# Optimization experiments

Measured on AMD Instinct MI355X. Metric: run time of the kernel, lower is better.

The kernel has to match this reference:

```python
import jax, jax.numpy as jnp
import numpy as np

HS = 1024      # hidden_size
NH = 16        # num_heads
HD = HS // NH  # head_dim = 64
WS = 24        # window_size
GWS = 8        # global_window_size
THETA = 10000.0
EPS = 1e-6


def _rope_tables():
    # matches Sam3ViTRotaryEmbedding with end_x=end_y=WS, scale=GWS/WS
    scale = GWS / WS
    freqs = 1.0 / THETA ** (np.arange(0, HD, 4)[: HD // 4].astype(np.float32) / HD)  # [HD//4]
    flat = np.arange(WS * WS)
    x_pos = (flat % WS).astype(np.float32) * scale
    y_pos = (flat // WS).astype(np.float32) * scale
    f = np.concatenate([np.outer(x_pos, freqs), np.outer(y_pos, freqs)], axis=-1)  # [S, HD//2]
    f = np.repeat(f, 2, axis=-1)  # repeat_interleave(2, dim=-1) -> [S, HD]
    return jnp.asarray(np.cos(f)), jnp.asarray(np.sin(f))


def _rotate_pairwise(x):
    shp = x.shape
    x = x.reshape(*shp[:-1], -1, 2)
    x1, x2 = x[..., 0], x[..., 1]
    return jnp.stack((-x2, x1), axis=-1).reshape(shp)


def _ln(x, g, b):
    m = x.mean(-1, keepdims=True)
    v = x.var(-1, keepdims=True)
    return (x - m) * jax.lax.rsqrt(v + EPS) * g + b


def setup_inputs() -> dict:
    key = jax.random.key(0)
    ks = jax.random.split(key, 8)
    B, H, W = 2, 72, 72
    s = 0.02
    inp = {
        "hidden_states": jax.random.normal(ks[0], (B, H, W, HS), jnp.float32),
        "ln1_g": jnp.ones((HS,), jnp.float32), "ln1_b": jnp.zeros((HS,), jnp.float32),
        "wq": jax.random.normal(ks[1], (HS, HS), jnp.float32) * s, "bq": jnp.zeros((HS,), jnp.float32),
        "wk": jax.random.normal(ks[2], (HS, HS), jnp.float32) * s, "bk": jnp.zeros((HS,), jnp.float32),
        "wv": jax.random.normal(ks[3], (HS, HS), jnp.float32) * s, "bv": jnp.zeros((HS,), jnp.float32),
        "wo": jax.random.normal(ks[4], (HS, HS), jnp.float32) * s, "bo": jnp.zeros((HS,), jnp.float32),
        "ln2_g": jnp.ones((HS,), jnp.float32), "ln2_b": jnp.zeros((HS,), jnp.float32),
        "w1": jax.random.normal(ks[5], (HS, 4 * HS), jnp.float32) * s, "b1": jnp.zeros((4 * HS,), jnp.float32),
        "w2": jax.random.normal(ks[6], (4 * HS, HS), jnp.float32) * s, "b2": jnp.zeros((HS,), jnp.float32),
    }
    return inp


def reference(hidden_states, ln1_g, ln1_b, wq, bq, wk, bk, wv, bv, wo, bo,
              ln2_g, ln2_b, w1, b1, w2, b2):
    B, H, W, C = hidden_states.shape
    residual = hidden_states
    x = _ln(hidden_states, ln1_g, ln1_b)

    # window partition: [B,H,W,C] -> [B*nW, S, C]  (H,W divisible by WS -> no pad)
    nh, nw = H // WS, W // WS
    xw = x.reshape(B, nh, WS, nw, WS, C).transpose(0, 1, 3, 2, 4, 5).reshape(-1, WS * WS, C)
    Bn, S = xw.shape[0], WS * WS

    q = (xw @ wq + bq).reshape(Bn, S, NH, HD).transpose(0, 2, 1, 3)  # [Bn,NH,S,HD]
    k = (xw @ wk + bk).reshape(Bn, S, NH, HD).transpose(0, 2, 1, 3)
    v = (xw @ wv + bv).reshape(Bn, S, NH, HD).transpose(0, 2, 1, 3)

    cos, sin = _rope_tables()  # [S, HD]
    q = q * cos + _rotate_pairwise(q) * sin
    k = k * cos + _rotate_pairwise(k) * sin

    attn = jax.nn.softmax(jnp.einsum('bhqd,bhkd->bhqk', q, k) * HD ** -0.5, axis=-1)
    o = jnp.einsum('bhqk,bhkd->bhqd', attn, v).transpose(0, 2, 1, 3).reshape(Bn, S, C)
    o = o @ wo + bo

    # window unpartition: [B*nW, S, C] -> [B,H,W,C]
    o = o.reshape(B, nh, nw, WS, WS, C).transpose(0, 1, 3, 2, 4, 5).reshape(B, H, W, C)

    x = residual + o
    y = _ln(x, ln2_g, ln2_b)
    y = jax.nn.gelu(y @ w1 + b1, approximate=False) @ w2 + b2
    return x + y
```

## Files before the change

kernel.cpp:

```cpp
#include <hip/hip_runtime.h>
#include <hip/hip_bf16.h>

#define DI __device__ __forceinline__

typedef short bf16x8 __attribute__((ext_vector_type(8)));
typedef float f32x4 __attribute__((ext_vector_type(4)));

typedef __attribute__((address_space(3))) unsigned lds_u32;
typedef __attribute__((address_space(1))) const unsigned g_u32;

DI void gload16(const void* g, void* lds) {
  __builtin_amdgcn_global_load_lds((g_u32*)g, (lds_u32*)lds, 16, 0, 0);
}

DI unsigned short bf16bits(float f) {
  __hip_bfloat16 h = __float2bfloat16(f);
  return *(unsigned short*)&h;
}

DI float gelu_fast(float v) {
  const float v2 = v * v;
  const float u = v * __builtin_fmaf(0.0356774081f, v2, 0.7978845608f);
  const float a = fabsf(u);
  const float e2 = __expf(-2.0f * a);
  const float r = __builtin_amdgcn_rcpf(1.0f + e2);
  float t = __builtin_fmaf(-2.0f * e2, r, 1.0f);
  t = copysignf(t, u);
  const float h = 0.5f * v;
  return __builtin_fmaf(h, t, h);
}

__global__ __launch_bounds__(256)
void wtrans_kernel(const float* __restrict__ w, __hip_bfloat16* __restrict__ wt,
                   int K, int N) {
  __shared__ float tile[32][33];
  const int nb = blockIdx.x * 32, kb = blockIdx.y * 32;
  const int tx = threadIdx.x & 31, ty = threadIdx.x >> 5;
#pragma unroll
  for (int i = 0; i < 4; ++i)
    tile[ty + i * 8][tx] = w[(size_t)(kb + ty + i * 8) * N + nb + tx];
  __syncthreads();
#pragma unroll
  for (int i = 0; i < 4; ++i)
    wt[(size_t)(nb + ty + i * 8) * K + kb + tx] = __float2bfloat16(tile[tx][ty + i * 8]);
}

__global__ void tables_kernel(float* __restrict__ cost, float* __restrict__ sint) {
  const int s = blockIdx.x;
  const int d = threadIdx.x;
  const int j = d >> 1;
  const float pos = (j < 16) ? (float)(s % 24) * (1.0f / 3.0f)
                             : (float)(s / 24) * (1.0f / 3.0f);
  const int fi = j & 15;
  const float freq = powf(10000.0f, -(float)fi * (1.0f / 16.0f));
  const float a = pos * freq;
  cost[s * 64 + d] = cosf(a);
  sint[s * 64 + d] = sinf(a);
}

__global__ __launch_bounds__(256)
void ln_kernel(const float* __restrict__ in, const float* __restrict__ g,
               const float* __restrict__ b, __hip_bfloat16* __restrict__ out) {
  const int t = blockIdx.x, tid = threadIdx.x;
  const float4 x = *(const float4*)(in + (size_t)t * 1024 + tid * 4);
  float s = x.x + x.y + x.z + x.w;
  float sq = x.x * x.x + x.y * x.y + x.z * x.z + x.w * x.w;
#pragma unroll
  for (int off = 32; off >= 1; off >>= 1) {
    s += __shfl_down(s, off);
    sq += __shfl_down(sq, off);
  }
  __shared__ float red[8];
  const int wave = tid >> 6, lane = tid & 63;
  if (lane == 0) { red[wave] = s; red[4 + wave] = sq; }
  __syncthreads();
  s = red[0] + red[1] + red[2] + red[3];
  sq = red[4] + red[5] + red[6] + red[7];
  const float mean = s * (1.0f / 1024.0f);
  const float var = sq * (1.0f / 1024.0f) - mean * mean;
  const float rstd = rsqrtf(var + 1e-6f);
  const int c = tid * 4;
  const float4 gg = *(const float4*)(g + c);
  const float4 bb = *(const float4*)(b + c);
  ushort4 o;
  o.x = bf16bits((x.x - mean) * rstd * gg.x + bb.x);
  o.y = bf16bits((x.y - mean) * rstd * gg.y + bb.y);
  o.z = bf16bits((x.z - mean) * rstd * gg.z + bb.z);
  o.w = bf16bits((x.w - mean) * rstd * gg.w + bb.w);
  *(ushort4*)((unsigned short*)out + (size_t)t * 1024 + c) = o;
}

template<int MODE>
__global__ __launch_bounds__(256)
void gemm_bt_kernel(const __hip_bfloat16* __restrict__ A,
                    const __hip_bfloat16* __restrict__ Bt,
                    const float* __restrict__ bias,
                    void* __restrict__ out,
                    const float* __restrict__ resid,
                    int M, int N, int K) {
  __shared__ __hip_bfloat16 As[128 * 64];
  __shared__ __hip_bfloat16 Bs[128 * 64];
  const int tid = threadIdx.x;
  const int wave = tid >> 6, lane = tid & 63;
  const int lr = lane & 15, lg = lane >> 4;
  const unsigned nwg = gridDim.x * gridDim.y;
  const unsigned bid0 = blockIdx.y * gridDim.x + blockIdx.x;
  const unsigned xcd = bid0 & 7u, idx = bid0 >> 3;
  const unsigned q8 = nwg >> 3, r8 = nwg & 7u;
  const unsigned L = (xcd < r8 ? xcd * (q8 + 1u)
                               : r8 * (q8 + 1u) + (xcd - r8) * q8) + idx;
  const unsigned gpr = gridDim.y * 8u;
  const unsigned grp = L / gpr, rr = L - grp * gpr;
  const int bm = (int)(rr >> 3) * 128;
  const int bn = (int)(grp * 8u + (rr & 7u)) * 128;
  const int wr = (wave >> 1) * 64, wc = (wave & 1) * 64;
  const int srow = lane >> 3;
  const int scol = ((lane & 7) ^ srow) * 8;
  const int rsw = lr & 7;

  f32x4 acc[4][4] = {};

  for (int k0 = 0; k0 < K; k0 += 64) {
#pragma unroll
    for (int c = 0; c < 4; ++c) {
      const int ch = wave * 4 + c;
      gload16(A + (size_t)(bm + ch * 8 + srow) * K + k0 + scol, &As[ch * 512]);
      gload16(Bt + (size_t)(bn + ch * 8 + srow) * K + k0 + scol, &Bs[ch * 512]);
    }
    __syncthreads();
#pragma unroll
    for (int kk = 0; kk < 64; kk += 32) {
      const int kg = kk >> 3;
      bf16x8 af[4], bfr[4];
#pragma unroll
      for (int i = 0; i < 4; ++i)
        af[i] = *(const bf16x8*)&As[(wr + i * 16 + lr) * 64 + (((kg + lg) ^ rsw) * 8)];
#pragma unroll
      for (int i = 0; i < 4; ++i)
        bfr[i] = *(const bf16x8*)&Bs[(wc + i * 16 + lr) * 64 + (((kg + lg) ^ rsw) * 8)];
#pragma unroll
      for (int mi = 0; mi < 4; ++mi)
#pragma unroll
        for (int ni = 0; ni < 4; ++ni)
          acc[mi][ni] = __builtin_amdgcn_mfma_f32_16x16x32_bf16(af[mi], bfr[ni],
                                                                acc[mi][ni], 0, 0, 0);
    }
    __syncthreads();
  }

#pragma unroll
  for (int ni = 0; ni < 4; ++ni) {
    const int gn = bn + wc + ni * 16 + lr;
    const float bv = bias ? bias[gn] : 0.0f;
#pragma unroll
    for (int mi = 0; mi < 4; ++mi) {
      const int rowb = bm + wr + mi * 16 + lg * 4;
#pragma unroll
      for (int j = 0; j < 4; ++j) {
        const float v = acc[mi][ni][j] + bv;
        const int gm = rowb + j;
        if (MODE == 0) {
          ((__hip_bfloat16*)out)[(size_t)gm * N + gn] = __float2bfloat16(v);
        } else if (MODE == 1) {
          const float gl = gelu_fast(v);
          ((__hip_bfloat16*)out)[(size_t)gm * N + gn] = __float2bfloat16(gl);
          __builtin_amdgcn_sched_barrier(0);
        } else if (MODE == 2) {
          ((float*)out)[(size_t)gm * N + gn] += v;
        } else {
          const int win = gm / 576, s = gm % 576;
          const int bb2 = win / 9, wi = (win % 9) / 3, wj = win % 3;
          const int t = (bb2 * 72 + wi * 24 + (s / 24)) * 72 + wj * 24 + (s % 24);
          ((float*)out)[(size_t)t * 1024 + gn] =
              resid[(size_t)t * 1024 + gn] + v;
        }
      }
    }
  }
}

__global__ __launch_bounds__(256)
void rope_kernel(const __hip_bfloat16* __restrict__ qkvraw,
                 const float* __restrict__ bq, const float* __restrict__ bk,
                 const float* __restrict__ cost, const float* __restrict__ sint,
                 __hip_bfloat16* __restrict__ qw, __hip_bfloat16* __restrict__ kw) {
  const int s = blockIdx.x;
  const int win = blockIdx.y;
  const int b = win / 9, wi = (win % 9) / 3, wj = win % 3;
  const int t = (b * 72 + wi * 24 + (s / 24)) * 72 + wj * 24 + (s % 24);
  const int tid = threadIdx.x;
  const int col = tid * 4;
  const int head = col >> 6, d = col & 63;
  const float c0 = cost[s * 64 + d + 0], c1 = cost[s * 64 + d + 1];
  const float c2 = cost[s * 64 + d + 2], c3 = cost[s * 64 + d + 3];
  const float s0 = sint[s * 64 + d + 0], s1 = sint[s * 64 + d + 1];
  const float s2 = sint[s * 64 + d + 2], s3 = sint[s * 64 + d + 3];
  const size_t rbase = (size_t)t * 3072;
  const size_t obase = (((size_t)(win * 16 + head)) * 576 + s) * 64 + d;
  {
    const float q0 = __bfloat162float(qkvraw[rbase + col + 0]) + bq[col + 0];
    const float q1 = __bfloat162float(qkvraw[rbase + col + 1]) + bq[col + 1];
    const float q2 = __bfloat162float(qkvraw[rbase + col + 2]) + bq[col + 2];
    const float q3 = __bfloat162float(qkvraw[rbase + col + 3]) + bq[col + 3];
    ushort4 o;
    o.x = bf16bits(0.125f * (q0 * c0 - q1 * s0));
    o.y = bf16bits(0.125f * (q1 * c1 + q0 * s1));
    o.z = bf16bits(0.125f * (q2 * c2 - q3 * s2));
    o.w = bf16bits(0.125f * (q3 * c3 + q2 * s3));
    *(ushort4*)((unsigned short*)qw + obase) = o;
  }
  {
    const float k0 = __bfloat162float(qkvraw[rbase + 1024 + col + 0]) + bk[col + 0];
    const float k1 = __bfloat162float(qkvraw[rbase + 1024 + col + 1]) + bk[col + 1];
    const float k2 = __bfloat162float(qkvraw[rbase + 1024 + col + 2]) + bk[col + 2];
    const float k3 = __bfloat162float(qkvraw[rbase + 1024 + col + 3]) + bk[col + 3];
    ushort4 o;
    o.x = bf16bits(k0 * c0 - k1 * s0);
    o.y = bf16bits(k1 * c1 + k0 * s1);
    o.z = bf16bits(k2 * c2 - k3 * s2);
    o.w = bf16bits(k3 * c3 + k2 * s3);
    *(ushort4*)((unsigned short*)kw + obase) = o;
  }
}

__global__ __launch_bounds__(256)
void vtrans_kernel(const __hip_bfloat16* __restrict__ qkvraw,
                   const float* __restrict__ bv,
                   __hip_bfloat16* __restrict__ vt) {
  const int head = blockIdx.x, win = blockIdx.y;
  const int b = win / 9, wi = (win % 9) / 3, wj = win % 3;
  __shared__ __hip_bfloat16 tile[64][72];
  const int tid = threadIdx.x;
  for (int s0 = 0; s0 < 576; s0 += 64) {
#pragma unroll
    for (int rep = 0; rep < 16; ++rep) {
      const int e = rep * 256 + tid;
      const int si = e >> 6, d = e & 63;
      const int s = s0 + si;
      const int t = (b * 72 + wi * 24 + (s / 24)) * 72 + wj * 24 + (s % 24);
      const float v = __bfloat162float(qkvraw[(size_t)t * 3072 + 2048 + head * 64 + d])
                    + bv[head * 64 + d];
      tile[d][si] = __float2bfloat16(v);
    }
    __syncthreads();
#pragma unroll
    for (int rep = 0; rep < 16; ++rep) {
      const int e = rep * 256 + tid;
      const int d = e >> 6, si = e & 63;
      vt[((size_t)(win * 16 + head) * 64 + d) * 576 + s0 + si] = tile[d][si];
    }
    __syncthreads();
  }
}

__global__ __launch_bounds__(256)
void attn_kernel(const __hip_bfloat16* __restrict__ qw,
                 const __hip_bfloat16* __restrict__ kw,
                 const __hip_bfloat16* __restrict__ vt,
                 __hip_bfloat16* __restrict__ ow) {
  __shared__ __hip_bfloat16 Klds[2][64 * 64];
  __shared__ __hip_bfloat16 Vlds[2][64 * 64];
  __shared__ __hip_bfloat16 Plds[4 * 16 * 64];
  const unsigned nwg = gridDim.x * gridDim.y * gridDim.z;
  const unsigned bid0 = (blockIdx.z * gridDim.y + blockIdx.y) * gridDim.x + blockIdx.x;
  const unsigned Lw = (bid0 & 7u) * (nwg >> 3) + (bid0 >> 3);
  const int qt = (int)(Lw % 9u);
  const unsigned r = Lw / 9u;
  const int head = (int)(r & 15u);
  const int win = (int)(r >> 4);
  const int bh = win * 16 + head;
  const int tid = threadIdx.x, wave = tid >> 6, lane = tid & 63;
  const int lr = lane & 15, lg = lane >> 4;
  const int rsw = lr & 7;

  const int qrow = qt * 64 + wave * 16 + lr;
  const __hip_bfloat16* qbase = qw + ((size_t)bh * 576 + qrow) * 64;
  const bf16x8 q0 = *(const bf16x8*)(qbase + lg * 8);
  const bf16x8 q1 = *(const bf16x8*)(qbase + 32 + lg * 8);

  f32x4 oacc[4] = {};
  float mrow[4] = {-1e30f, -1e30f, -1e30f, -1e30f};
  float lrow[4] = {};

  const int srow = lane >> 3;
  const int sw = ((lane & 7) ^ srow) * 8;

  auto stagekv = [&](int buf, int kv) {
#pragma unroll
    for (int c = 0; c < 2; ++c) {
      const int ch = wave * 2 + c;
      gload16(kw + ((size_t)bh * 576 + kv * 64 + ch * 8 + srow) * 64 + sw,
              &Klds[buf][ch * 512]);
      gload16(vt + ((size_t)bh * 64 + ch * 8 + srow) * 576 + kv * 64 + sw,
              &Vlds[buf][ch * 512]);
    }
  };

  stagekv(0, 0);
  __syncthreads();

  for (int kv = 0; kv < 9; ++kv) {
    const int cur = kv & 1;
    if (kv + 1 < 9) stagekv(cur ^ 1, kv + 1);
    __builtin_amdgcn_sched_barrier(0);

    f32x4 sfr[4];
    __builtin_amdgcn_s_setprio(1);
#pragma unroll
    for (int c = 0; c < 4; ++c) {
      const bf16x8 b0 = *(const bf16x8*)&Klds[cur][(c * 16 + lr) * 64 + ((lg ^ rsw) * 8)];
      const bf16x8 b1 = *(const bf16x8*)&Klds[cur][(c * 16 + lr) * 64 + (((4 + lg) ^ rsw) * 8)];
      f32x4 z = {};
      z = __builtin_amdgcn_mfma_f32_16x16x32_bf16(q0, b0, z, 0, 0, 0);
      z = __builtin_amdgcn_mfma_f32_16x16x32_bf16(q1, b1, z, 0, 0, 0);
      sfr[c] = z;
    }
    __builtin_amdgcn_s_setprio(0);

    float p[4][4], rscale[4];
#pragma unroll
    for (int j = 0; j < 4; ++j) {
      float mj = fmaxf(fmaxf(sfr[0][j], sfr[1][j]), fmaxf(sfr[2][j], sfr[3][j]));
#pragma unroll
      for (int off = 1; off < 16; off <<= 1) mj = fmaxf(mj, __shfl_xor(mj, off));
      const float mn = fmaxf(mrow[j], mj);
      rscale[j] = __expf(mrow[j] - mn);
      mrow[j] = mn;
      float rs = 0.0f;
#pragma unroll
      for (int c = 0; c < 4; ++c) {
        const float pp = __expf(sfr[c][j] - mn);
        p[c][j] = pp;
        rs += pp;
      }
#pragma unroll
      for (int off = 1; off < 16; off <<= 1) rs += __shfl_xor(rs, off);
      lrow[j] = lrow[j] * rscale[j] + rs;
    }
#pragma unroll
    for (int d = 0; d < 4; ++d)
#pragma unroll
      for (int j = 0; j < 4; ++j) oacc[d][j] *= rscale[j];

    {
      const int g0 = lr >> 3, c3 = lr & 7;
#pragma unroll
      for (int c = 0; c < 4; ++c)
#pragma unroll
        for (int j = 0; j < 4; ++j) {
          const int row = lg * 4 + j;
          const int g = (c * 2 + g0) ^ (row & 7);
          Plds[wave * 1024 + row * 64 + g * 8 + c3] = __float2bfloat16(p[c][j]);
        }
    }

    const bf16x8 pa0 = *(const bf16x8*)&Plds[wave * 1024 + lr * 64 + ((lg ^ rsw) * 8)];
    const bf16x8 pa1 = *(const bf16x8*)&Plds[wave * 1024 + lr * 64 + (((4 + lg) ^ rsw) * 8)];
    __builtin_amdgcn_s_setprio(1);
#pragma unroll
    for (int d = 0; d < 4; ++d) {
      const bf16x8 v0 = *(const bf16x8*)&Vlds[cur][(d * 16 + lr) * 64 + ((lg ^ rsw) * 8)];
      const bf16x8 v1 = *(const bf16x8*)&Vlds[cur][(d * 16 + lr) * 64 + (((4 + lg) ^ rsw) * 8)];
      oacc[d] = __builtin_amdgcn_mfma_f32_16x16x32_bf16(pa0, v0, oacc[d], 0, 0, 0);
      oacc[d] = __builtin_amdgcn_mfma_f32_16x16x32_bf16(pa1, v1, oacc[d], 0, 0, 0);
    }
    __builtin_amdgcn_s_setprio(0);
    __syncthreads();
  }

#pragma unroll
  for (int j = 0; j < 4; ++j) {
    const float inv = 1.0f / lrow[j];
    const int srow2 = qt * 64 + wave * 16 + lg * 4 + j;
    const size_t base = ((size_t)win * 576 + srow2) * 1024 + head * 64;
#pragma unroll
    for (int d = 0; d < 4; ++d)
      ow[base + d * 16 + lr] = __float2bfloat16(oacc[d][j] * inv);
  }
}

extern "C" void kernel_launch(void* const* d_in, const int* in_sizes, int n_in,
                              void* d_out, int out_size, void* d_ws, size_t ws_size,
                              hipStream_t stream) {
  const float* hidden = (const float*)d_in[0];
  const float* ln1_g = (const float*)d_in[1];
  const float* ln1_b = (const float*)d_in[2];
  const float* wq = (const float*)d_in[3];
  const float* bq = (const float*)d_in[4];
  const float* wk = (const float*)d_in[5];
  const float* bk = (const float*)d_in[6];
  const float* wv = (const float*)d_in[7];
  const float* bv = (const float*)d_in[8];
  const float* wo = (const float*)d_in[9];
  const float* bo = (const float*)d_in[10];
  const float* ln2_g = (const float*)d_in[11];
  const float* ln2_b = (const float*)d_in[12];
  const float* w1 = (const float*)d_in[13];
  const float* b1 = (const float*)d_in[14];
  const float* w2 = (const float*)d_in[15];
  const float* b2 = (const float*)d_in[16];
  float* out = (float*)d_out;

  char* p = (char*)d_ws;
  auto alloc = [&](size_t bytes) {
    char* r = p;
    p += (bytes + 255) & ~(size_t)255;
    return r;
  };
  __hip_bfloat16* wt_qkv = (__hip_bfloat16*)alloc(3072ull * 1024 * 2);
  __hip_bfloat16* wt_wo  = (__hip_bfloat16*)alloc(1024ull * 1024 * 2);
  __hip_bfloat16* wt_w1  = (__hip_bfloat16*)alloc(4096ull * 1024 * 2);
  __hip_bfloat16* wt_w2  = (__hip_bfloat16*)alloc(1024ull * 4096 * 2);
  float* cost = (float*)alloc(576ull * 64 * 4);
  float* sint = (float*)alloc(576ull * 64 * 4);
  __hip_bfloat16* xbuf = (__hip_bfloat16*)alloc(10368ull * 1024 * 2);
  char* big = alloc(10368ull * 4096 * 2);
  __hip_bfloat16* qkvraw = (__hip_bfloat16*)big;
  __hip_bfloat16* qw = (__hip_bfloat16*)(big + 10368ull * 3072 * 2);
  __hip_bfloat16* h1 = (__hip_bfloat16*)big;
  __hip_bfloat16* kw = (__hip_bfloat16*)alloc(18ull * 16 * 576 * 64 * 2);
  __hip_bfloat16* vt = (__hip_bfloat16*)alloc(18ull * 16 * 64 * 576 * 2);

  wtrans_kernel<<<dim3(32, 32), 256, 0, stream>>>(wq, wt_qkv, 1024, 1024);
  wtrans_kernel<<<dim3(32, 32), 256, 0, stream>>>(wk, wt_qkv + 1024ull * 1024, 1024, 1024);
  wtrans_kernel<<<dim3(32, 32), 256, 0, stream>>>(wv, wt_qkv + 2048ull * 1024, 1024, 1024);
  wtrans_kernel<<<dim3(32, 32), 256, 0, stream>>>(wo, wt_wo, 1024, 1024);
  wtrans_kernel<<<dim3(128, 32), 256, 0, stream>>>(w1, wt_w1, 1024, 4096);
  wtrans_kernel<<<dim3(32, 128), 256, 0, stream>>>(w2, wt_w2, 4096, 1024);
  tables_kernel<<<576, 64, 0, stream>>>(cost, sint);

  ln_kernel<<<10368, 256, 0, stream>>>(hidden, ln1_g, ln1_b, xbuf);
  gemm_bt_kernel<0><<<dim3(24, 81), 256, 0, stream>>>(
      xbuf, wt_qkv, nullptr, qkvraw, nullptr, 10368, 3072, 1024);
  rope_kernel<<<dim3(576, 18), 256, 0, stream>>>(qkvraw, bq, bk, cost, sint, qw, kw);
  vtrans_kernel<<<dim3(16, 18), 256, 0, stream>>>(qkvraw, bv, vt);
  attn_kernel<<<dim3(9, 16, 18), 256, 0, stream>>>(qw, kw, vt, xbuf);
  gemm_bt_kernel<3><<<dim3(8, 81), 256, 0, stream>>>(
      xbuf, wt_wo, bo, out, hidden, 10368, 1024, 1024);
  ln_kernel<<<10368, 256, 0, stream>>>(out, ln2_g, ln2_b, xbuf);
  gemm_bt_kernel<1><<<dim3(32, 81), 256, 0, stream>>>(
      xbuf, wt_w1, b1, h1, nullptr, 10368, 4096, 1024);
  gemm_bt_kernel<2><<<dim3(8, 81), 256, 0, stream>>>(
      h1, wt_w2, b2, out, nullptr, 10368, 1024, 4096);
}
```

Baseline: 561.7 us.

## Merge prep kernels, fuse rope with V transpose, add lazy softmax rescaling

```diff
diff --git a/kernel.cpp b/kernel.cpp
--- a/kernel.cpp
+++ b/kernel.cpp
@@ -31,31 +31,53 @@
 }
 
 __global__ __launch_bounds__(256)
-void wtrans_kernel(const float* __restrict__ w, __hip_bfloat16* __restrict__ wt,
-                   int K, int N) {
-  __shared__ float tile[32][33];
-  const int nb = blockIdx.x * 32, kb = blockIdx.y * 32;
+void prep_kernel(const float* __restrict__ wq, const float* __restrict__ wk,
+                 const float* __restrict__ wv, const float* __restrict__ wo,
+                 const float* __restrict__ w1, const float* __restrict__ w2,
+                 __hip_bfloat16* __restrict__ wt_qkv,
+                 __hip_bfloat16* __restrict__ wt_wo,
+                 __hip_bfloat16* __restrict__ wt_w1,
+                 __hip_bfloat16* __restrict__ wt_w2,
+                 float* __restrict__ cost, float* __restrict__ sint) {
+  const int idx = blockIdx.x;
+  if (idx >= 12288) {
+    const int e = (idx - 12288) * 4 + (threadIdx.x >> 6);
+    const int d = threadIdx.x & 63;
+    const int j = d >> 1;
+    const float pos = (j < 16) ? (float)(e % 24) * (1.0f / 3.0f)
+                               : (float)(e / 24) * (1.0f / 3.0f);
+    const int fi = j & 15;
+    const float freq = powf(10000.0f, -(float)fi * (1.0f / 16.0f));
+    const float a = pos * freq;
+    cost[e * 64 + d] = cosf(a);
+    sint[e * 64 + d] = sinf(a);
+    return;
+  }
+  const float* w;
+  __hip_bfloat16* wt;
+  int K, N, tile;
+  if (idx < 4096) {
+    const int seg = idx >> 10;
+    tile = idx & 1023;
+    K = 1024; N = 1024;
+    w = (seg == 0) ? wq : (seg == 1) ? wk : (seg == 2) ? wv : wo;
+    wt = (seg < 3) ? (wt_qkv + (size_t)seg * 1024 * 1024) : wt_wo;
+  } else if (idx < 8192) {
+    tile = idx - 4096; K = 1024; N = 4096; w = w1; wt = wt_w1;
+  } else {
+    tile = idx - 8192; K = 4096; N = 1024; w = w2; wt = wt_w2;
+  }
+  const int ntx = N >> 5;
+  const int nb = (tile % ntx) * 32, kb = (tile / ntx) * 32;
+  __shared__ float tilebuf[32][33];
   const int tx = threadIdx.x & 31, ty = threadIdx.x >> 5;
 #pragma unroll
   for (int i = 0; i < 4; ++i)
-    tile[ty + i * 8][tx] = w[(size_t)(kb + ty + i * 8) * N + nb + tx];
+    tilebuf[ty + i * 8][tx] = w[(size_t)(kb + ty + i * 8) * N + nb + tx];
   __syncthreads();
 #pragma unroll
   for (int i = 0; i < 4; ++i)
-    wt[(size_t)(nb + ty + i * 8) * K + kb + tx] = __float2bfloat16(tile[tx][ty + i * 8]);
-}
-
-__global__ void tables_kernel(float* __restrict__ cost, float* __restrict__ sint) {
-  const int s = blockIdx.x;
-  const int d = threadIdx.x;
-  const int j = d >> 1;
-  const float pos = (j < 16) ? (float)(s % 24) * (1.0f / 3.0f)
-                             : (float)(s / 24) * (1.0f / 3.0f);
-  const int fi = j & 15;
-  const float freq = powf(10000.0f, -(float)fi * (1.0f / 16.0f));
-  const float a = pos * freq;
-  cost[s * 64 + d] = cosf(a);
-  sint[s * 64 + d] = sinf(a);
+    wt[(size_t)(nb + ty + i * 8) * K + kb + tx] = __float2bfloat16(tilebuf[tx][ty + i * 8]);
 }
 
 __global__ __launch_bounds__(256)
@@ -180,57 +202,54 @@
 }
 
 __global__ __launch_bounds__(256)
-void rope_kernel(const __hip_bfloat16* __restrict__ qkvraw,
-                 const float* __restrict__ bq, const float* __restrict__ bk,
-                 const float* __restrict__ cost, const float* __restrict__ sint,
-                 __hip_bfloat16* __restrict__ qw, __hip_bfloat16* __restrict__ kw) {
-  const int s = blockIdx.x;
+void ropev_kernel(const __hip_bfloat16* __restrict__ qkvraw,
+                  const float* __restrict__ bq, const float* __restrict__ bk,
+                  const float* __restrict__ bv,
+                  const float* __restrict__ cost, const float* __restrict__ sint,
+                  __hip_bfloat16* __restrict__ qw, __hip_bfloat16* __restrict__ kw,
+                  __hip_bfloat16* __restrict__ vt) {
+  __shared__ __hip_bfloat16 tile[64][72];
   const int win = blockIdx.y;
   const int b = win / 9, wi = (win % 9) / 3, wj = win % 3;
-  const int t = (b * 72 + wi * 24 + (s / 24)) * 72 + wj * 24 + (s % 24);
   const int tid = threadIdx.x;
-  const int col = tid * 4;
-  const int head = col >> 6, d = col & 63;
-  const float c0 = cost[s * 64 + d + 0], c1 = cost[s * 64 + d + 1];
-  const float c2 = cost[s * 64 + d + 2], c3 = cost[s * 64 + d + 3];
-  const float s0 = sint[s * 64 + d + 0], s1 = sint[s * 64 + d + 1];
-  const float s2 = sint[s * 64 + d + 2], s3 = sint[s * 64 + d + 3];
-  const size_t rbase = (size_t)t * 3072;
-  const size_t obase = (((size_t)(win * 16 + head)) * 576 + s) * 64 + d;
-  {
-    const float q0 = __bfloat162float(qkvraw[rbase + col + 0]) + bq[col + 0];
-    const float q1 = __bfloat162float(qkvraw[rbase + col + 1]) + bq[col + 1];
-    const float q2 = __bfloat162float(qkvraw[rbase + col + 2]) + bq[col + 2];
-    const float q3 = __bfloat162float(qkvraw[rbase + col + 3]) + bq[col + 3];
-    ushort4 o;
-    o.x = bf16bits(0.125f * (q0 * c0 - q1 * s0));
-    o.y = bf16bits(0.125f * (q1 * c1 + q0 * s1));
-    o.z = bf16bits(0.125f * (q2 * c2 - q3 * s2));
-    o.w = bf16bits(0.125f * (q3 * c3 + q2 * s3));
-    *(ushort4*)((unsigned short*)qw + obase) = o;
-  }
-  {
-    const float k0 = __bfloat162float(qkvraw[rbase + 1024 + col + 0]) + bk[col + 0];
-    const float k1 = __bfloat162float(qkvraw[rbase + 1024 + col + 1]) + bk[col + 1];
-    const float k2 = __bfloat162float(qkvraw[rbase + 1024 + col + 2]) + bk[col + 2];
-    const float k3 = __bfloat162float(qkvraw[rbase + 1024 + col + 3]) + bk[col + 3];
-    ushort4 o;
-    o.x = bf16bits(k0 * c0 - k1 * s0);
-    o.y = bf16bits(k1 * c1 + k0 * s1);
-    o.z = bf16bits(k2 * c2 - k3 * s2);
-    o.w = bf16bits(k3 * c3 + k2 * s3);
-    *(ushort4*)((unsigned short*)kw + obase) = o;
-  }
-}
-
-__global__ __launch_bounds__(256)
-void vtrans_kernel(const __hip_bfloat16* __restrict__ qkvraw,
-                   const float* __restrict__ bv,
-                   __hip_bfloat16* __restrict__ vt) {
-  const int head = blockIdx.x, win = blockIdx.y;
-  const int b = win / 9, wi = (win % 9) / 3, wj = win % 3;
-  __shared__ __hip_bfloat16 tile[64][72];
-  const int tid = threadIdx.x;
+  if (blockIdx.x < 576) {
+    const int s = blockIdx.x;
+    const int t = (b * 72 + wi * 24 + (s / 24)) * 72 + wj * 24 + (s % 24);
+    const int col = tid * 4;
+    const int head = col >> 6, d = col & 63;
+    const float c0 = cost[s * 64 + d + 0], c1 = cost[s * 64 + d + 1];
+    const float c2 = cost[s * 64 + d + 2], c3 = cost[s * 64 + d + 3];
+    const float s0 = sint[s * 64 + d + 0], s1 = sint[s * 64 + d + 1];
+    const float s2 = sint[s * 64 + d + 2], s3 = sint[s * 64 + d + 3];
+    const size_t rbase = (size_t)t * 3072;
+    const size_t obase = (((size_t)(win * 16 + head)) * 576 + s) * 64 + d;
+    {
+      const float q0 = __bfloat162float(qkvraw[rbase + col + 0]) + bq[col + 0];
+      const float q1 = __bfloat162float(qkvraw[rbase + col + 1]) + bq[col + 1];
+      const float q2 = __bfloat162float(qkvraw[rbase + col + 2]) + bq[col + 2];
+      const float q3 = __bfloat162float(qkvraw[rbase + col + 3]) + bq[col + 3];
+      ushort4 o;
+      o.x = bf16bits(0.125f * (q0 * c0 - q1 * s0));
+      o.y = bf16bits(0.125f * (q1 * c1 + q0 * s1));
+      o.z = bf16bits(0.125f * (q2 * c2 - q3 * s2));
+      o.w = bf16bits(0.125f * (q3 * c3 + q2 * s3));
+      *(ushort4*)((unsigned short*)qw + obase) = o;
+    }
+    {
+      const float k0 = __bfloat162float(qkvraw[rbase + 1024 + col + 0]) + bk[col + 0];
+      const float k1 = __bfloat162float(qkvraw[rbase + 1024 + col + 1]) + bk[col + 1];
+      const float k2 = __bfloat162float(qkvraw[rbase + 1024 + col + 2]) + bk[col + 2];
+      const float k3 = __bfloat162float(qkvraw[rbase + 1024 + col + 3]) + bk[col + 3];
+      ushort4 o;
+      o.x = bf16bits(k0 * c0 - k1 * s0);
+      o.y = bf16bits(k1 * c1 + k0 * s1);
+      o.z = bf16bits(k2 * c2 - k3 * s2);
+      o.w = bf16bits(k3 * c3 + k2 * s3);
+      *(ushort4*)((unsigned short*)kw + obase) = o;
+    }
+    return;
+  }
+  const int head = blockIdx.x - 576;
   for (int s0 = 0; s0 < 576; s0 += 64) {
 #pragma unroll
     for (int rep = 0; rep < 16; ++rep) {
@@ -317,30 +336,42 @@
     }
     __builtin_amdgcn_s_setprio(0);
 
-    float p[4][4], rscale[4];
+    float mjv[4];
 #pragma unroll
     for (int j = 0; j < 4; ++j) {
       float mj = fmaxf(fmaxf(sfr[0][j], sfr[1][j]), fmaxf(sfr[2][j], sfr[3][j]));
 #pragma unroll
       for (int off = 1; off < 16; off <<= 1) mj = fmaxf(mj, __shfl_xor(mj, off));
-      const float mn = fmaxf(mrow[j], mj);
-      rscale[j] = __expf(mrow[j] - mn);
-      mrow[j] = mn;
+      mjv[j] = mj;
+    }
+    bool defer = true;
+#pragma unroll
+    for (int j = 0; j < 4; ++j) defer = defer && (mjv[j] <= mrow[j] + 8.0f);
+    if (!__all(defer)) {
+#pragma unroll
+      for (int j = 0; j < 4; ++j) {
+        const float mn = fmaxf(mrow[j], mjv[j]);
+        const float rs = __expf(mrow[j] - mn);
+        mrow[j] = mn;
+        lrow[j] *= rs;
+#pragma unroll
+        for (int d = 0; d < 4; ++d) oacc[d][j] *= rs;
+      }
+    }
+    float p[4][4];
+#pragma unroll
+    for (int j = 0; j < 4; ++j) {
       float rs = 0.0f;
 #pragma unroll
       for (int c = 0; c < 4; ++c) {
-        const float pp = __expf(sfr[c][j] - mn);
+        const float pp = __expf(sfr[c][j] - mrow[j]);
         p[c][j] = pp;
         rs += pp;
       }
 #pragma unroll
       for (int off = 1; off < 16; off <<= 1) rs += __shfl_xor(rs, off);
-      lrow[j] = lrow[j] * rscale[j] + rs;
-    }
-#pragma unroll
-    for (int d = 0; d < 4; ++d)
-#pragma unroll
-      for (int j = 0; j < 4; ++j) oacc[d][j] *= rscale[j];
+      lrow[j] += rs;
+    }
 
     {
       const int g0 = lr >> 3, c3 = lr & 7;
@@ -421,19 +452,13 @@
   __hip_bfloat16* kw = (__hip_bfloat16*)alloc(18ull * 16 * 576 * 64 * 2);
   __hip_bfloat16* vt = (__hip_bfloat16*)alloc(18ull * 16 * 64 * 576 * 2);
 
-  wtrans_kernel<<<dim3(32, 32), 256, 0, stream>>>(wq, wt_qkv, 1024, 1024);
-  wtrans_kernel<<<dim3(32, 32), 256, 0, stream>>>(wk, wt_qkv + 1024ull * 1024, 1024, 1024);
-  wtrans_kernel<<<dim3(32, 32), 256, 0, stream>>>(wv, wt_qkv + 2048ull * 1024, 1024, 1024);
-  wtrans_kernel<<<dim3(32, 32), 256, 0, stream>>>(wo, wt_wo, 1024, 1024);
-  wtrans_kernel<<<dim3(128, 32), 256, 0, stream>>>(w1, wt_w1, 1024, 4096);
-  wtrans_kernel<<<dim3(32, 128), 256, 0, stream>>>(w2, wt_w2, 4096, 1024);
-  tables_kernel<<<576, 64, 0, stream>>>(cost, sint);
-
+  prep_kernel<<<12432, 256, 0, stream>>>(wq, wk, wv, wo, w1, w2,
+                                         wt_qkv, wt_wo, wt_w1, wt_w2, cost, sint);
   ln_kernel<<<10368, 256, 0, stream>>>(hidden, ln1_g, ln1_b, xbuf);
   gemm_bt_kernel<0><<<dim3(24, 81), 256, 0, stream>>>(
       xbuf, wt_qkv, nullptr, qkvraw, nullptr, 10368, 3072, 1024);
-  rope_kernel<<<dim3(576, 18), 256, 0, stream>>>(qkvraw, bq, bk, cost, sint, qw, kw);
-  vtrans_kernel<<<dim3(16, 18), 256, 0, stream>>>(qkvraw, bv, vt);
+  ropev_kernel<<<dim3(592, 18), 256, 0, stream>>>(
+      qkvraw, bq, bk, bv, cost, sint, qw, kw, vt);
   attn_kernel<<<dim3(9, 16, 18), 256, 0, stream>>>(qw, kw, vt, xbuf);
   gemm_bt_kernel<3><<<dim3(8, 81), 256, 0, stream>>>(
       xbuf, wt_wo, bo, out, hidden, 10368, 1024, 1024);
```

New measurement: 551.5 us, median of 2. No clear change (-1.8%).
